# Kernel optimization log

Hardware: AMD Instinct MI355X
Metric: run time of the kernel (lower is better)

Reference implementation:

```python
import jax, jax.numpy as jnp
import numpy as np

B, T, I, H = 2048, 4096, 5, 10  # batch, seq_len, input_dim, hidden_dim


def setup_inputs() -> dict:
    key = jax.random.key(0)
    ks = jax.random.split(key, 5)
    return {
        "x": jax.random.normal(ks[0], (B, T, I), dtype=jnp.float32),
        "h0": jnp.zeros((1, B, H), dtype=jnp.float32),
        "c0": jnp.zeros((1, B, H), dtype=jnp.float32),
        "W_ih": jax.random.normal(ks[1], (4 * H, I), dtype=jnp.float32) * 0.3,
        "W_hh": jax.random.normal(ks[2], (4 * H, H), dtype=jnp.float32) * 0.3,
        "b_ih": jax.random.normal(ks[3], (4 * H,), dtype=jnp.float32) * 0.1,
        "b_hh": jax.random.normal(ks[4], (4 * H,), dtype=jnp.float32) * 0.1,
    }


def reference(x, h0, c0, W_ih, W_hh, b_ih, b_hh):
    # Single-layer nn.LSTM (batch_first=True), gate order i,f,g,o.
    # Precompute input contribution for all timesteps: [B,T,4H]
    x_gates = jnp.einsum("bti,gi->btg", x, W_ih) + b_ih + b_hh

    def step(carry, xg_t):
        h, c = carry  # [B,H] each
        gates = xg_t + h @ W_hh.T  # [B,4H]
        i_g, f_g, g_g, o_g = jnp.split(gates, 4, axis=-1)
        i_g = jax.nn.sigmoid(i_g)
        f_g = jax.nn.sigmoid(f_g)
        g_g = jnp.tanh(g_g)
        o_g = jax.nn.sigmoid(o_g)
        c = f_g * c + i_g * g_g
        h = o_g * jnp.tanh(c)
        return (h, c), h

    (_, _), hs = jax.lax.scan(step, (h0[0], c0[0]), jnp.swapaxes(x_gates, 0, 1))
    return jnp.swapaxes(hs, 0, 1)  # [B,T,H], matching lstm_out
```

## Files before the change

kernel.cpp:

```cpp
#include <hip/hip_runtime.h>


#define BB 2048
#define TT 4096
#define II 5
#define HH 10
#define CH 256
#define CHF (CH * II)
#define PSTRIDE 32
#define BUFB (CH * PSTRIDE)
#define NCHUNK (TT / CH)

__device__ __forceinline__ float readlane_f(float v, int l) {
    union { float f; int i; } u;
    u.f = v;
    u.i = __builtin_amdgcn_readlane(u.i, l);
    return u.f;
}

template<int E>
__device__ __forceinline__ float quad_bcast(float v) {
    union { float f; int i; } u;
    u.f = v;
    u.i = __builtin_amdgcn_update_dpp(u.i, u.i, E * 0x55, 0xF, 0xF, false);
    return u.f;
}

__global__ __launch_bounds__(64) void lstm_wave_kernel(
    const float* __restrict__ x,
    const float* __restrict__ h0,
    const float* __restrict__ c0,
    const float* __restrict__ W_ih,
    const float* __restrict__ W_hh,
    const float* __restrict__ b_ih,
    const float* __restrict__ b_hh,
    float* __restrict__ out)
{
    __shared__ __align__(16) char xs[2][BUFB];

    const int b = blockIdx.x;
    const int lane = threadIdx.x;
    const int j = lane >> 2;
    const int k = lane & 3;
    const bool active = (lane < 4 * HH);

    const float LOG2E = 1.4426950408889634f;
    const float KC = -2.f * LOG2E;
    const float scale = (k == 2) ? KC : -LOG2E;

    float wih[II];
    float whh[HH];
    float bias = 0.f;
    if (active) {
        const int row = k * HH + j;
#pragma unroll
        for (int q = 0; q < II; q++) wih[q] = W_ih[row * II + q] * scale;
#pragma unroll
        for (int q = 0; q < HH; q++) whh[q] = W_hh[row * HH + q] * scale;
        bias = (b_ih[row] + b_hh[row]) * scale;
    } else {
#pragma unroll
        for (int q = 0; q < II; q++) wih[q] = 0.f;
#pragma unroll
        for (int q = 0; q < HH; q++) whh[q] = 0.f;
    }

    const float am = (k == 2) ? (2.f * KC) : 1.f;
    const float ac = (k == 2) ? (-KC) : 0.f;

    float hval = 0.f, cs = 0.f;
    if (active) {
        hval = h0[b * HH + j];
        cs   = c0[b * HH + j] * KC;
    }

    const float* xrow = x + (size_t)b * TT * II;

    float* outp = out + (size_t)b * TT * HH + k * HH + j;

    int wa[II][4];
#pragma unroll
    for (int q = 0; q < II; q++) {
#pragma unroll
        for (int c4 = 0; c4 < 4; c4++) {
            const int p = (q * 64 + lane) * 4 + c4;
            wa[q][c4] = (p / II) * PSTRIDE + (p % II) * 4;
        }
    }

    float4 pf[II];
    {
        const float4* xv = (const float4*)xrow;
#pragma unroll
        for (int q = 0; q < II; q++) pf[q] = xv[q * 64 + lane];
        char* dst = xs[0];
#pragma unroll
        for (int q = 0; q < II; q++) {
            *(float*)(dst + wa[q][0]) = pf[q].x;
            *(float*)(dst + wa[q][1]) = pf[q].y;
            *(float*)(dst + wa[q][2]) = pf[q].z;
            *(float*)(dst + wa[q][3]) = pf[q].w;
        }
    }

    float keep = 0.f;

    for (int c = 0; c < NCHUNK; ++c) {
        const char* xc = xs[c & 1];

        if (c + 1 < NCHUNK) {
            const float4* xv = (const float4*)(xrow + (size_t)(c + 1) * CHF);
#pragma unroll
            for (int q = 0; q < II; q++) pf[q] = xv[q * 64 + lane];
        }

#pragma unroll 8
        for (int u = 0; u < CH; ++u) {
            const float4 xv4 = *(const float4*)(xc + u * PSTRIDE);
            const float x4v  = *(const float*)(xc + u * PSTRIDE + 16);

            float a0 = fmaf(xv4.x, wih[0], bias);
            float a1 = xv4.y * wih[1];
            float a2 = xv4.z * wih[2];
            float a3 = xv4.w * wih[3];
            a0 = fmaf(x4v, wih[4], a0);

            a0 = fmaf(readlane_f(hval, 0),  whh[0], a0);
            a1 = fmaf(readlane_f(hval, 4),  whh[1], a1);
            a2 = fmaf(readlane_f(hval, 8),  whh[2], a2);
            a3 = fmaf(readlane_f(hval, 12), whh[3], a3);
            a0 = fmaf(readlane_f(hval, 16), whh[4], a0);
            a1 = fmaf(readlane_f(hval, 20), whh[5], a1);
            a2 = fmaf(readlane_f(hval, 24), whh[6], a2);
            a3 = fmaf(readlane_f(hval, 28), whh[7], a3);
            a0 = fmaf(readlane_f(hval, 32), whh[8], a0);
            a1 = fmaf(readlane_f(hval, 36), whh[9], a1);
            const float acc = (a0 + a1) + (a2 + a3);

            const float e = __builtin_amdgcn_exp2f(acc);
            const float s = __builtin_amdgcn_rcpf(1.f + e);
            const float act = fmaf(s, am, ac);

            const float iv = quad_bcast<0>(act);
            const float fv = quad_bcast<1>(act);
            const float gs = quad_bcast<2>(act);
            const float ov = quad_bcast<3>(act);

            cs = fmaf(fv, cs, iv * gs);
            const float e2 = __builtin_amdgcn_exp2f(cs);
            const float th = fmaf(__builtin_amdgcn_rcpf(1.f + e2), 2.f, -1.f);
            hval = ov * th;

            keep = ((u & 3) == k) ? hval : keep;
            if ((u & 3) == 3) {
                const int off = ((u & 7) == 3) ? 0 : 40;
                if (active) outp[off] = keep;
            }
            if ((u & 7) == 7) outp += 80;
        }

        if (c + 1 < NCHUNK) {
            char* dst = xs[(c + 1) & 1];
#pragma unroll
            for (int q = 0; q < II; q++) {
                *(float*)(dst + wa[q][0]) = pf[q].x;
                *(float*)(dst + wa[q][1]) = pf[q].y;
                *(float*)(dst + wa[q][2]) = pf[q].z;
                *(float*)(dst + wa[q][3]) = pf[q].w;
            }
        }
    }
}

extern "C" void kernel_launch(void* const* d_in, const int* in_sizes, int n_in,
                              void* d_out, int out_size, void* d_ws, size_t ws_size,
                              hipStream_t stream) {
    const float* x    = (const float*)d_in[0];
    const float* h0   = (const float*)d_in[1];
    const float* c0   = (const float*)d_in[2];
    const float* W_ih = (const float*)d_in[3];
    const float* W_hh = (const float*)d_in[4];
    const float* b_ih = (const float*)d_in[5];
    const float* b_hh = (const float*)d_in[6];
    float* out = (float*)d_out;

    lstm_wave_kernel<<<dim3(BB), dim3(64), 0, stream>>>(
        x, h0, c0, W_ih, W_hh, b_ih, b_hh, out);
}
```

Measured before the change: 1.059 ms.

## Process two batch rows per wave to interleave independent recurrences

Each 64-lane wave now runs the LSTM recurrence for two batch elements at once, interleaving their dependent chains of readlanes, exp/rcp and DPP broadcasts so the latency of one can be hidden by the other. The shared-memory staging layout is widened so both rows' inputs for a timestep sit together and load as vector reads. The grid is halved to 1024 waves, which cuts available parallelism across CUs, and the per-step instruction count roughly doubles, raising register pressure.

```diff
diff --git a/kernel.cpp b/kernel.cpp
--- a/kernel.cpp
+++ b/kernel.cpp
@@ -7,7 +7,7 @@
 #define HH 10
 #define CH 256
 #define CHF (CH * II)
-#define PSTRIDE 32
+#define PSTRIDE 48
 #define BUFB (CH * PSTRIDE)
 #define NCHUNK (TT / CH)
 
@@ -26,7 +26,7 @@
     return u.f;
 }
 
-__global__ __launch_bounds__(64) void lstm_wave_kernel(
+__global__ __launch_bounds__(64, 1) void lstm_wave_kernel(
     const float* __restrict__ x,
     const float* __restrict__ h0,
     const float* __restrict__ c0,
@@ -36,9 +36,11 @@
     const float* __restrict__ b_hh,
     float* __restrict__ out)
 {
-    __shared__ __align__(16) char xs[2][BUFB];
-
-    const int b = blockIdx.x;
+    __shared__ __align__(16) char xs[2 * BUFB];
+
+    const int blk = blockIdx.x;
+    const int b0 = 2 * blk;
+    const int b1 = b0 + 1;
     const int lane = threadIdx.x;
     const int j = lane >> 2;
     const int k = lane & 3;
@@ -68,15 +70,19 @@
     const float am = (k == 2) ? (2.f * KC) : 1.f;
     const float ac = (k == 2) ? (-KC) : 0.f;
 
-    float hval = 0.f, cs = 0.f;
+    float hA = 0.f, csA = 0.f, hB = 0.f, csB = 0.f;
     if (active) {
-        hval = h0[b * HH + j];
-        cs   = c0[b * HH + j] * KC;
-    }
-
-    const float* xrow = x + (size_t)b * TT * II;
-
-    float* outp = out + (size_t)b * TT * HH + k * HH + j;
+        hA  = h0[b0 * HH + j];
+        csA = c0[b0 * HH + j] * KC;
+        hB  = h0[b1 * HH + j];
+        csB = c0[b1 * HH + j] * KC;
+    }
+
+    const float* xrowA = x + (size_t)b0 * TT * II;
+    const float* xrowB = x + (size_t)b1 * TT * II;
+
+    float* outpA = out + (size_t)b0 * TT * HH + k * HH + j;
+    float* outpB = out + (size_t)b1 * TT * HH + k * HH + j;
 
     int wa[II][4];
 #pragma unroll
@@ -84,89 +90,142 @@
 #pragma unroll
         for (int c4 = 0; c4 < 4; c4++) {
             const int p = (q * 64 + lane) * 4 + c4;
-            wa[q][c4] = (p / II) * PSTRIDE + (p % II) * 4;
-        }
-    }
-
-    float4 pf[II];
+            wa[q][c4] = (p / II) * PSTRIDE + (p % II) * 8;
+        }
+    }
+
+    float4 pfA[II], pfB[II];
     {
-        const float4* xv = (const float4*)xrow;
-#pragma unroll
-        for (int q = 0; q < II; q++) pf[q] = xv[q * 64 + lane];
-        char* dst = xs[0];
+        const float4* xvA = (const float4*)xrowA;
+        const float4* xvB = (const float4*)xrowB;
 #pragma unroll
         for (int q = 0; q < II; q++) {
-            *(float*)(dst + wa[q][0]) = pf[q].x;
-            *(float*)(dst + wa[q][1]) = pf[q].y;
-            *(float*)(dst + wa[q][2]) = pf[q].z;
-            *(float*)(dst + wa[q][3]) = pf[q].w;
-        }
-    }
-
-    float keep = 0.f;
+            pfA[q] = xvA[q * 64 + lane];
+            pfB[q] = xvB[q * 64 + lane];
+        }
+        char* dst = xs;
+#pragma unroll
+        for (int q = 0; q < II; q++) {
+            *(float*)(dst + wa[q][0])     = pfA[q].x;
+            *(float*)(dst + wa[q][1])     = pfA[q].y;
+            *(float*)(dst + wa[q][2])     = pfA[q].z;
+            *(float*)(dst + wa[q][3])     = pfA[q].w;
+            *(float*)(dst + wa[q][0] + 4) = pfB[q].x;
+            *(float*)(dst + wa[q][1] + 4) = pfB[q].y;
+            *(float*)(dst + wa[q][2] + 4) = pfB[q].z;
+            *(float*)(dst + wa[q][3] + 4) = pfB[q].w;
+        }
+    }
+
+    float keepA = 0.f, keepB = 0.f;
 
     for (int c = 0; c < NCHUNK; ++c) {
-        const char* xc = xs[c & 1];
+        const char* xc = xs + (c & 1) * BUFB;
 
         if (c + 1 < NCHUNK) {
-            const float4* xv = (const float4*)(xrow + (size_t)(c + 1) * CHF);
-#pragma unroll
-            for (int q = 0; q < II; q++) pf[q] = xv[q * 64 + lane];
+            const float4* xvA = (const float4*)(xrowA + (size_t)(c + 1) * CHF);
+            const float4* xvB = (const float4*)(xrowB + (size_t)(c + 1) * CHF);
+#pragma unroll
+            for (int q = 0; q < II; q++) {
+                pfA[q] = xvA[q * 64 + lane];
+                pfB[q] = xvB[q * 64 + lane];
+            }
         }
 
 #pragma unroll 8
         for (int u = 0; u < CH; ++u) {
-            const float4 xv4 = *(const float4*)(xc + u * PSTRIDE);
-            const float x4v  = *(const float*)(xc + u * PSTRIDE + 16);
-
-            float a0 = fmaf(xv4.x, wih[0], bias);
-            float a1 = xv4.y * wih[1];
-            float a2 = xv4.z * wih[2];
-            float a3 = xv4.w * wih[3];
-            a0 = fmaf(x4v, wih[4], a0);
-
-            a0 = fmaf(readlane_f(hval, 0),  whh[0], a0);
-            a1 = fmaf(readlane_f(hval, 4),  whh[1], a1);
-            a2 = fmaf(readlane_f(hval, 8),  whh[2], a2);
-            a3 = fmaf(readlane_f(hval, 12), whh[3], a3);
-            a0 = fmaf(readlane_f(hval, 16), whh[4], a0);
-            a1 = fmaf(readlane_f(hval, 20), whh[5], a1);
-            a2 = fmaf(readlane_f(hval, 24), whh[6], a2);
-            a3 = fmaf(readlane_f(hval, 28), whh[7], a3);
-            a0 = fmaf(readlane_f(hval, 32), whh[8], a0);
-            a1 = fmaf(readlane_f(hval, 36), whh[9], a1);
-            const float acc = (a0 + a1) + (a2 + a3);
-
-            const float e = __builtin_amdgcn_exp2f(acc);
-            const float s = __builtin_amdgcn_rcpf(1.f + e);
-            const float act = fmaf(s, am, ac);
-
-            const float iv = quad_bcast<0>(act);
-            const float fv = quad_bcast<1>(act);
-            const float gs = quad_bcast<2>(act);
-            const float ov = quad_bcast<3>(act);
-
-            cs = fmaf(fv, cs, iv * gs);
-            const float e2 = __builtin_amdgcn_exp2f(cs);
-            const float th = fmaf(__builtin_amdgcn_rcpf(1.f + e2), 2.f, -1.f);
-            hval = ov * th;
-
-            keep = ((u & 3) == k) ? hval : keep;
+            const char* xp = xc + u * PSTRIDE;
+            const float4 r0 = *(const float4*)(xp);
+            const float4 r1 = *(const float4*)(xp + 16);
+            const float2 r2 = *(const float2*)(xp + 32);
+
+            float aA0 = fmaf(r0.x, wih[0], bias);
+            float aB0 = fmaf(r0.y, wih[0], bias);
+            float aA1 = r0.z * wih[1];
+            float aB1 = r0.w * wih[1];
+            float aA2 = r1.x * wih[2];
+            float aB2 = r1.y * wih[2];
+            float aA3 = r1.z * wih[3];
+            float aB3 = r1.w * wih[3];
+            aA0 = fmaf(r2.x, wih[4], aA0);
+            aB0 = fmaf(r2.y, wih[4], aB0);
+
+            aA0 = fmaf(readlane_f(hA, 0),  whh[0], aA0);
+            aA1 = fmaf(readlane_f(hA, 4),  whh[1], aA1);
+            aA2 = fmaf(readlane_f(hA, 8),  whh[2], aA2);
+            aA3 = fmaf(readlane_f(hA, 12), whh[3], aA3);
+            aA0 = fmaf(readlane_f(hA, 16), whh[4], aA0);
+            aA1 = fmaf(readlane_f(hA, 20), whh[5], aA1);
+            aA2 = fmaf(readlane_f(hA, 24), whh[6], aA2);
+            aA3 = fmaf(readlane_f(hA, 28), whh[7], aA3);
+            aA0 = fmaf(readlane_f(hA, 32), whh[8], aA0);
+            aA1 = fmaf(readlane_f(hA, 36), whh[9], aA1);
+            const float accA = (aA0 + aA1) + (aA2 + aA3);
+
+            aB0 = fmaf(readlane_f(hB, 0),  whh[0], aB0);
+            aB1 = fmaf(readlane_f(hB, 4),  whh[1], aB1);
+            aB2 = fmaf(readlane_f(hB, 8),  whh[2], aB2);
+            aB3 = fmaf(readlane_f(hB, 12), whh[3], aB3);
+            aB0 = fmaf(readlane_f(hB, 16), whh[4], aB0);
+            aB1 = fmaf(readlane_f(hB, 20), whh[5], aB1);
+            aB2 = fmaf(readlane_f(hB, 24), whh[6], aB2);
+            aB3 = fmaf(readlane_f(hB, 28), whh[7], aB3);
+            aB0 = fmaf(readlane_f(hB, 32), whh[8], aB0);
+            aB1 = fmaf(readlane_f(hB, 36), whh[9], aB1);
+            const float accB = (aB0 + aB1) + (aB2 + aB3);
+
+            const float eA = __builtin_amdgcn_exp2f(accA);
+            const float eB = __builtin_amdgcn_exp2f(accB);
+            const float sA = __builtin_amdgcn_rcpf(1.f + eA);
+            const float sB = __builtin_amdgcn_rcpf(1.f + eB);
+            const float actA = fmaf(sA, am, ac);
+            const float actB = fmaf(sB, am, ac);
+
+            const float ivA = quad_bcast<0>(actA);
+            const float fvA = quad_bcast<1>(actA);
+            const float gsA = quad_bcast<2>(actA);
+            const float ovA = quad_bcast<3>(actA);
+            const float ivB = quad_bcast<0>(actB);
+            const float fvB = quad_bcast<1>(actB);
+            const float gsB = quad_bcast<2>(actB);
+            const float ovB = quad_bcast<3>(actB);
+
+            csA = fmaf(fvA, csA, ivA * gsA);
+            csB = fmaf(fvB, csB, ivB * gsB);
+            const float e2A = __builtin_amdgcn_exp2f(csA);
+            const float e2B = __builtin_amdgcn_exp2f(csB);
+            const float thA = fmaf(__builtin_amdgcn_rcpf(1.f + e2A), 2.f, -1.f);
+            const float thB = fmaf(__builtin_amdgcn_rcpf(1.f + e2B), 2.f, -1.f);
+            hA = ovA * thA;
+            hB = ovB * thB;
+
+            keepA = ((u & 3) == k) ? hA : keepA;
+            keepB = ((u & 3) == k) ? hB : keepB;
             if ((u & 3) == 3) {
                 const int off = ((u & 7) == 3) ? 0 : 40;
-                if (active) outp[off] = keep;
-            }
-            if ((u & 7) == 7) outp += 80;
+                if (active) {
+                    outpA[off] = keepA;
+                    outpB[off] = keepB;
+                }
+            }
+            if ((u & 7) == 7) {
+                outpA += 80;
+                outpB += 80;
+            }
         }
 
         if (c + 1 < NCHUNK) {
-            char* dst = xs[(c + 1) & 1];
+            char* dst = xs + ((c + 1) & 1) * BUFB;
 #pragma unroll
             for (int q = 0; q < II; q++) {
-                *(float*)(dst + wa[q][0]) = pf[q].x;
-                *(float*)(dst + wa[q][1]) = pf[q].y;
-                *(float*)(dst + wa[q][2]) = pf[q].z;
-                *(float*)(dst + wa[q][3]) = pf[q].w;
+                *(float*)(dst + wa[q][0])     = pfA[q].x;
+                *(float*)(dst + wa[q][1])     = pfA[q].y;
+                *(float*)(dst + wa[q][2])     = pfA[q].z;
+                *(float*)(dst + wa[q][3])     = pfA[q].w;
+                *(float*)(dst + wa[q][0] + 4) = pfB[q].x;
+                *(float*)(dst + wa[q][1] + 4) = pfB[q].y;
+                *(float*)(dst + wa[q][2] + 4) = pfB[q].z;
+                *(float*)(dst + wa[q][3] + 4) = pfB[q].w;
             }
         }
     }
@@ -184,6 +243,6 @@
     const float* b_hh = (const float*)d_in[6];
     float* out = (float*)d_out;
 
-    lstm_wave_kernel<<<dim3(BB), dim3(64), 0, stream>>>(
+    lstm_wave_kernel<<<dim3(BB / 2), dim3(64), 0, stream>>>(
         x, h0, c0, W_ih, W_hh, b_ih, b_hh, out);
 }
```

Result: slower. 1.152 ms (+8.9%).
